# Kernel tuning notes

Hardware: AMD Instinct MI355X
Metric: run time of the kernel (lower is better)

The kernel has to match this reference:

```python
import jax, jax.numpy as jnp
import numpy as np

N = 100000   # nodes
E = 1000000  # edges
F = 128      # num_features
H = 64       # hidden_size
C = 1        # num_classes
G = 128      # num graphs in batch


def gcn_conv(x, W, b, src, dst, deg_inv_sqrt):
    # PyG GCNConv: add self-loops, symmetric normalization D^-1/2 (A+I) D^-1/2, then X W + b
    h = x @ W                                   # [N, H]
    norm = deg_inv_sqrt[src] * deg_inv_sqrt[dst]  # [E]
    msg = h[src] * norm[:, None]                # gather + scale, [E, H]
    out = jnp.zeros_like(h).at[dst].add(msg)    # scatter-add to targets
    out = out + h * (deg_inv_sqrt ** 2)[:, None]  # self-loop contribution
    return out + b


def setup_inputs() -> dict:
    key = jax.random.key(0)
    ks = jax.random.split(key, 12)
    x = jax.random.normal(ks[0], (N, F), dtype=jnp.float32)
    edge_index = jax.random.randint(ks[1], (2, E), 0, N, dtype=jnp.int32).astype(jnp.int64)
    batch = jnp.sort(jax.random.randint(ks[2], (N,), 0, G, dtype=jnp.int32)).astype(jnp.int64)
    def glorot(k, fan_in, fan_out):
        s = np.float32(np.sqrt(6.0 / (fan_in + fan_out)))
        return jax.random.uniform(k, (fan_in, fan_out), jnp.float32, -s, s)
    return {
        "x": x, "edge_index": edge_index, "batch": batch,
        "W1": glorot(ks[3], F, H), "b1": jnp.zeros((H,), jnp.float32),
        "W2": glorot(ks[4], H, H), "b2": jnp.zeros((H,), jnp.float32),
        "Wl1": glorot(ks[5], H, H), "bl1": jnp.zeros((H,), jnp.float32),
        "Wl2": glorot(ks[6], H, C), "bl2": jnp.zeros((C,), jnp.float32),
    }


def reference(x, edge_index, batch, W1, b1, W2, b2, Wl1, bl1, Wl2, bl2):
    src, dst = edge_index[0], edge_index[1]
    # degree with self-loops: 1 + in-degree(target)
    deg = jnp.ones((N,), x.dtype).at[dst].add(jnp.ones((E,), x.dtype))
    deg_inv_sqrt = jax.lax.rsqrt(deg)
    h = jax.nn.relu(gcn_conv(x, W1, b1, src, dst, deg_inv_sqrt))
    h = jax.nn.relu(gcn_conv(h, W2, b2, src, dst, deg_inv_sqrt))
    g = jax.ops.segment_sum(h, batch, num_segments=G)  # global_add_pool, [G, H]
    g = jax.nn.relu(g @ Wl1 + bl1)
    out = g @ Wl2 + bl2                                # [G, 1]
    return out.squeeze(axis=1)                         # [G]
```

## Files before the change

kernel.cpp:

```cpp
#include <hip/hip_runtime.h>

#define NN 100000
#define EE 1000000
#define FF 128
#define HH 64
#define GG 128
#define NB 391
#define MMB 1563
#define GCB 2048

__device__ inline unsigned short f2bf(float f) {
    unsigned u = __float_as_uint(f);
    u += 0x7fffu + ((u >> 16) & 1u);
    return (unsigned short)(u >> 16);
}
__device__ inline float bf2f(unsigned short h) {
    return __uint_as_float((unsigned)h << 16);
}

__global__ void k_hist(const int* __restrict__ ei, int* __restrict__ cnt) {
    int e = blockIdx.x * 256 + threadIdx.x;
    if (e < EE) atomicAdd(&cnt[ei[EE + e]], 1);
}

__global__ void k_scan1(const int* __restrict__ cnt, int* __restrict__ part,
                        float* __restrict__ dis) {
    int i = blockIdx.x * 256 + threadIdx.x;
    int c = (i < NN) ? cnt[i] : 0;
    if (i < NN) dis[i] = rsqrtf((float)(c + 1));
    int v = (i < NN) ? c : 0;
    for (int o = 1; o < 64; o <<= 1) v += __shfl_xor(v, o);
    __shared__ int ws[4];
    if ((threadIdx.x & 63) == 0) ws[threadIdx.x >> 6] = v;
    __syncthreads();
    if (threadIdx.x == 0) part[blockIdx.x] = ws[0] + ws[1] + ws[2] + ws[3];
}

__global__ void k_scan2(int* __restrict__ part) {
    __shared__ int buf[512];
    int t = threadIdx.x;
    int v = (t < NB) ? part[t] : 0;
    buf[t] = v; __syncthreads();
    for (int o = 1; o < 512; o <<= 1) {
        int u = (t >= o) ? buf[t - o] : 0;
        __syncthreads();
        buf[t] += u;
        __syncthreads();
    }
    if (t < NB) part[t] = buf[t] - v;
}

__global__ void k_scan3(const int* __restrict__ cnt, const int* __restrict__ part,
                        int* __restrict__ row_ptr, int* __restrict__ cursor) {
    int i = blockIdx.x * 256 + threadIdx.x;
    int v = (i < NN) ? cnt[i] : 0;
    int lane = threadIdx.x & 63, w = threadIdx.x >> 6;
    int incl = v;
    for (int o = 1; o < 64; o <<= 1) { int u = __shfl_up(incl, o); if (lane >= o) incl += u; }
    __shared__ int ws[4];
    if (lane == 63) ws[w] = incl;
    __syncthreads();
    int woff = 0;
    for (int k = 0; k < w; ++k) woff += ws[k];
    int excl = incl - v + woff + part[blockIdx.x];
    if (i < NN) {
        row_ptr[i] = excl;
        cursor[i]  = excl;
    }
    if (i == 0) row_ptr[NN] = EE;
}

template<int K, int XBF>
__device__ __forceinline__ void
mm_body(const void* __restrict__ Xv, const float* __restrict__ W,
        const float* __restrict__ dis, unsigned* __restrict__ Y8,
        float* __restrict__ S, float* __restrict__ Wl, int bid) {
    for (int i = threadIdx.x; i < K * HH; i += 256) Wl[i] = W[i];
    __syncthreads();
    const int lane = threadIdx.x & 63;
    const int wv   = threadIdx.x >> 6;
    const int c4   = (lane & 15) * 4;
    const int rsg  = lane >> 4;
    const int r0   = bid * 64 + wv * 16 + rsg * 4;

    const char* Xb = (const char*)Xv;
    const size_t rb = (size_t)K * (XBF ? 2 : 4);
    const char* xr0; const char* xr1; const char* xr2; const char* xr3;
    {
        int a = r0, b_ = r0 + 1, c = r0 + 2, d = r0 + 3;
        if (a > NN - 1) a = NN - 1;
        if (b_ > NN - 1) b_ = NN - 1;
        if (c > NN - 1) c = NN - 1;
        if (d > NN - 1) d = NN - 1;
        xr0 = Xb + (size_t)a * rb; xr1 = Xb + (size_t)b_ * rb;
        xr2 = Xb + (size_t)c * rb; xr3 = Xb + (size_t)d * rb;
    }
    float4 acc0 = {0,0,0,0}, acc1 = {0,0,0,0}, acc2 = {0,0,0,0}, acc3 = {0,0,0,0};

#pragma unroll 8
    for (int k4 = 0; k4 < K / 4; ++k4) {
        float4 x0, x1, x2, x3;
        if (XBF) {
            ushort4 u0 = *(const ushort4*)(xr0 + k4 * 8);
            ushort4 u1 = *(const ushort4*)(xr1 + k4 * 8);
            ushort4 u2 = *(const ushort4*)(xr2 + k4 * 8);
            ushort4 u3 = *(const ushort4*)(xr3 + k4 * 8);
            x0 = {bf2f(u0.x), bf2f(u0.y), bf2f(u0.z), bf2f(u0.w)};
            x1 = {bf2f(u1.x), bf2f(u1.y), bf2f(u1.z), bf2f(u1.w)};
            x2 = {bf2f(u2.x), bf2f(u2.y), bf2f(u2.z), bf2f(u2.w)};
            x3 = {bf2f(u3.x), bf2f(u3.y), bf2f(u3.z), bf2f(u3.w)};
        } else {
            x0 = *(const float4*)(xr0 + k4 * 16);
            x1 = *(const float4*)(xr1 + k4 * 16);
            x2 = *(const float4*)(xr2 + k4 * 16);
            x3 = *(const float4*)(xr3 + k4 * 16);
        }
        const float4 w0 = *(const float4*)&Wl[(k4 * 4 + 0) * HH + c4];
        const float4 w1 = *(const float4*)&Wl[(k4 * 4 + 1) * HH + c4];
        const float4 w2 = *(const float4*)&Wl[(k4 * 4 + 2) * HH + c4];
        const float4 w3 = *(const float4*)&Wl[(k4 * 4 + 3) * HH + c4];
#define FMA4(A, XS) \
        A.x = fmaf(XS.x, w0.x, A.x); A.y = fmaf(XS.x, w0.y, A.y); \
        A.z = fmaf(XS.x, w0.z, A.z); A.w = fmaf(XS.x, w0.w, A.w); \
        A.x = fmaf(XS.y, w1.x, A.x); A.y = fmaf(XS.y, w1.y, A.y); \
        A.z = fmaf(XS.y, w1.z, A.z); A.w = fmaf(XS.y, w1.w, A.w); \
        A.x = fmaf(XS.z, w2.x, A.x); A.y = fmaf(XS.z, w2.y, A.y); \
        A.z = fmaf(XS.z, w2.z, A.z); A.w = fmaf(XS.z, w2.w, A.w); \
        A.x = fmaf(XS.w, w3.x, A.x); A.y = fmaf(XS.w, w3.y, A.y); \
        A.z = fmaf(XS.w, w3.z, A.z); A.w = fmaf(XS.w, w3.w, A.w);
        FMA4(acc0, x0) FMA4(acc1, x1) FMA4(acc2, x2) FMA4(acc3, x3)
#undef FMA4
    }
#define STORE(I, A) { \
        const int r = r0 + I; \
        if (r < NN) { \
            const float d = dis[r]; \
            const float ax = A.x * d, ay = A.y * d, az = A.z * d, aw = A.w * d; \
            float m = fmaxf(fmaxf(fabsf(ax), fabsf(ay)), fmaxf(fabsf(az), fabsf(aw))); \
            m = fmaxf(m, __shfl_xor(m, 1)); m = fmaxf(m, __shfl_xor(m, 2)); \
            m = fmaxf(m, __shfl_xor(m, 4)); m = fmaxf(m, __shfl_xor(m, 8)); \
            const float inv = 127.0f / m; \
            int q0 = __float2int_rn(ax * inv), q1 = __float2int_rn(ay * inv); \
            int q2 = __float2int_rn(az * inv), q3 = __float2int_rn(aw * inv); \
            if (m == 0.0f) { q0 = q1 = q2 = q3 = 0; } \
            const unsigned pk = (q0 & 0xff) | ((q1 & 0xff) << 8) | \
                                ((q2 & 0xff) << 16) | ((q3 & 0xff) << 24); \
            Y8[(size_t)r * 16 + (c4 >> 2)] = pk; \
            if (c4 == 0) S[r] = m * (1.0f / 127.0f); \
        } }
    STORE(0, acc0) STORE(1, acc1) STORE(2, acc2) STORE(3, acc3)
#undef STORE
}

template<int K, int XBF>
__global__ __launch_bounds__(256) void
k_matmul_b(const void* __restrict__ X, const float* __restrict__ W,
           const float* __restrict__ dis, unsigned* __restrict__ Y8,
           float* __restrict__ S) {
    __shared__ float Wl[K * HH];
    mm_body<K, XBF>(X, W, dis, Y8, S, Wl, blockIdx.x);
}

__global__ __launch_bounds__(256) void
k_mm1_place(const float* __restrict__ X, const float* __restrict__ W,
            const float* __restrict__ dis, unsigned* __restrict__ Y8,
            float* __restrict__ S, const int* __restrict__ ei,
            int* __restrict__ cursor, int* __restrict__ srcs) {
    __shared__ float Wl[FF * HH];
    if (blockIdx.x < MMB) {
        mm_body<FF, 0>(X, W, dis, Y8, S, Wl, blockIdx.x);
    } else {
        int e = (blockIdx.x - MMB) * 256 + threadIdx.x;
        if (e < EE) {
            int d = ei[EE + e];
            int p = atomicAdd(&cursor[d], 1);
            srcs[p] = ei[e];
        }
    }
}

template<bool POOL>
__global__ __launch_bounds__(256) void
k_gconv(const int* __restrict__ row_ptr, const int* __restrict__ srcs,
        const float* __restrict__ dis, const unsigned* __restrict__ H8,
        const float* __restrict__ S, const float* __restrict__ b,
        unsigned short* __restrict__ Out, const int* __restrict__ batch,
        float* __restrict__ g) {
    const int lane = threadIdx.x & 63;
    const int li   = lane & 15;
    const int qr   = lane >> 4;
    const float bl = b[lane];

    for (int node = blockIdx.x * 4 + (threadIdx.x >> 6); node < NN; node += GCB * 4) {
        const int p0   = row_ptr[node];
        const int deg  = row_ptr[node + 1] - p0;
        const int nbatch = (deg + 8) >> 3;

        float ac0 = 0.f, ac1 = 0.f, ac2 = 0.f, ac3 = 0.f;

#define IDX(bi, dA, dB) { \
        const int iA = 8 * (bi) + qr, iB = iA + 4; \
        dA = __builtin_nontemporal_load(srcs + p0 + (iA < deg ? iA : 0)); \
        dB = __builtin_nontemporal_load(srcs + p0 + (iB < deg ? iB : 0)); }
#define VAL(bi, sA, sB, vA, vB, gA, gB) { \
        const int iA = 8 * (bi) + qr, iB = iA + 4; \
        const int rA = (iA < deg) ? sA : node; \
        const int rB = (iB < deg) ? sB : node; \
        vA = H8[(size_t)rA * 16 + li];  gA = S[rA]; \
        vB = H8[(size_t)rB * 16 + li];  gB = S[rB]; }
#define CONSUME(bi, vA, vB, gA, gB) { \
        const int iA = 8 * (bi) + qr, iB = iA + 4; \
        const float s0 = (iA <= deg) ? gA : 0.f; \
        const float s1 = (iB <= deg) ? gB : 0.f; \
        ac0 = fmaf(s0, (float)(signed char)(vA      ), ac0); \
        ac1 = fmaf(s0, (float)(signed char)(vA >> 8 ), ac1); \
        ac2 = fmaf(s0, (float)(signed char)(vA >> 16), ac2); \
        ac3 = fmaf(s0, (float)(signed char)(vA >> 24), ac3); \
        ac0 = fmaf(s1, (float)(signed char)(vB      ), ac0); \
        ac1 = fmaf(s1, (float)(signed char)(vB >> 8 ), ac1); \
        ac2 = fmaf(s1, (float)(signed char)(vB >> 16), ac2); \
        ac3 = fmaf(s1, (float)(signed char)(vB >> 24), ac3); }

        int sA0, sA1, sB0, sB1;
        unsigned vA0, vA1;
        float gA0, gA1;
        IDX(0, sA0, sA1);
        VAL(0, sA0, sA1, vA0, vA1, gA0, gA1);
        IDX(1, sB0, sB1);
        for (int bi = 1; bi < nbatch; ++bi) {
            unsigned vB0, vB1;
            float gB0, gB1;
            VAL(bi, sB0, sB1, vB0, vB1, gB0, gB1);
            IDX(bi + 1, sB0, sB1);
            CONSUME(bi - 1, vA0, vA1, gA0, gA1);
            vA0 = vB0; vA1 = vB1; gA0 = gB0; gA1 = gB1;
        }
        CONSUME(nbatch - 1, vA0, vA1, gA0, gA1);
#undef IDX
#undef VAL
#undef CONSUME

        ac0 += __shfl_xor(ac0, 16); ac0 += __shfl_xor(ac0, 32);
        ac1 += __shfl_xor(ac1, 16); ac1 += __shfl_xor(ac1, 32);
        ac2 += __shfl_xor(ac2, 16); ac2 += __shfl_xor(ac2, 32);
        ac3 += __shfl_xor(ac3, 16); ac3 += __shfl_xor(ac3, 32);
        const float c0 = __shfl(ac0, lane >> 2);
        const float c1 = __shfl(ac1, lane >> 2);
        const float c2 = __shfl(ac2, lane >> 2);
        const float c3 = __shfl(ac3, lane >> 2);
        const int m = lane & 3;
        const float acc = (m == 0) ? c0 : (m == 1) ? c1 : (m == 2) ? c2 : c3;

        float v = acc * dis[node] + bl;
        v = fmaxf(v, 0.0f);
        if (POOL) {
            unsafeAtomicAdd(&g[(size_t)batch[node] * HH + lane], v);
        } else {
            __builtin_nontemporal_store(f2bf(v), Out + (size_t)node * HH + lane);
        }
    }
}

__global__ void k_head1(const float* __restrict__ g, const float* __restrict__ W,
                        const float* __restrict__ b, float* __restrict__ g2) {
    const int idx = blockIdx.x * 256 + threadIdx.x;
    const int row = idx >> 6;
    const int col = idx & 63;
    const float* gr = g + (size_t)row * HH;
    float acc = b[col];
#pragma unroll
    for (int k = 0; k < HH; ++k) acc = fmaf(gr[k], W[k * HH + col], acc);
    g2[idx] = acc > 0.0f ? acc : 0.0f;
}

__global__ void k_head2(const float* __restrict__ g2, const float* __restrict__ W,
                        const float* __restrict__ b, float* __restrict__ out) {
    const int r = threadIdx.x;
    if (r >= GG) return;
    const float* gr = g2 + (size_t)r * HH;
    float acc = 0.0f;
#pragma unroll
    for (int k = 0; k < HH; ++k) acc = fmaf(gr[k], W[k], acc);
    out[r] = acc + b[0];
}

extern "C" void kernel_launch(void* const* d_in, const int* in_sizes, int n_in,
                              void* d_out, int out_size, void* d_ws, size_t ws_size,
                              hipStream_t stream) {
    const float* x   = (const float*)d_in[0];
    const int*   ei  = (const int*)d_in[1];
    const int*   bat = (const int*)d_in[2];
    const float* W1  = (const float*)d_in[3];
    const float* b1  = (const float*)d_in[4];
    const float* W2  = (const float*)d_in[5];
    const float* b2  = (const float*)d_in[6];
    const float* Wl1 = (const float*)d_in[7];
    const float* bl1 = (const float*)d_in[8];
    const float* Wl2 = (const float*)d_in[9];
    const float* bl2 = (const float*)d_in[10];
    float* out = (float*)d_out;

    char* w = (char*)d_ws;
    float*    dis     = (float*)(w);
    int*      cnt     = (int*)  (w + 400128);
    int*      row_ptr = (int*)  (w + 800256);
    int*      cursor  = (int*)  (w + 1200640);
    int*      part    = (int*)  (w + 1600768);
    int*      srcs    = (int*)  (w + 1602816);
    float*    S       = (float*)(w + 5602816);
    unsigned* H8      = (unsigned*)(w + 6002944);
    unsigned short* A = (unsigned short*)(w + 12402944);
    float*    g       = (float*)(w + 25202944);
    float*    g2      = g + GG * HH;

    hipMemsetAsync(cnt, 0, (size_t)NN * sizeof(int), stream);
    k_hist <<<(EE + 255) / 256, 256, 0, stream>>>(ei, cnt);
    k_scan1<<<NB, 256, 0, stream>>>(cnt, part, dis);
    k_scan2<<<1, 512, 0, stream>>>(part);
    k_scan3<<<NB, 256, 0, stream>>>(cnt, part, row_ptr, cursor);

    k_mm1_place<<<MMB + (EE + 255) / 256, 256, 0, stream>>>(x, W1, dis, H8, S, ei, cursor, srcs);
    k_gconv<false><<<GCB, 256, 0, stream>>>(row_ptr, srcs, dis, H8, S, b1, A, nullptr, nullptr);

    k_matmul_b<HH, 1><<<MMB, 256, 0, stream>>>(A, W2, dis, H8, S);
    hipMemsetAsync(g, 0, (size_t)GG * HH * sizeof(float), stream);
    k_gconv<true><<<GCB, 256, 0, stream>>>(row_ptr, srcs, dis, H8, S, b2, nullptr, bat, g);

    k_head1<<<(GG * HH) / 256, 256, 0, stream>>>(g, Wl1, bl1, g2);
    k_head2<<<1, 128, 0, stream>>>(g2, Wl2, bl2, out);
}
```

Baseline: 280.0 us.

## Split fused matmul/placement kernel and K-tile weights in shared memory

Un-fuses the first matmul from the edge placement pass so each runs as its own kernel, and tiles the weight matrix into 64-row chunks in shared memory (16 KB instead of 32 KB for K=128), which should allow more blocks per CU. It also replaces nontemporal loads/stores in the gather-conv kernel with ordinary cached accesses. The cost is an extra launch, lost overlap between the placement atomics and the matmul, and an extra pair of barriers per K-chunk.

```diff
diff --git a/kernel.cpp b/kernel.cpp
--- a/kernel.cpp
+++ b/kernel.cpp
@@ -70,18 +70,27 @@
     if (i == 0) row_ptr[NN] = EE;
 }
 
+__global__ void k_place(const int* __restrict__ ei, int* __restrict__ cursor,
+                        int* __restrict__ srcs) {
+    int e = blockIdx.x * 256 + threadIdx.x;
+    if (e < EE) {
+        int d = ei[EE + e];
+        int p = atomicAdd(&cursor[d], 1);
+        srcs[p] = ei[e];
+    }
+}
+
 template<int K, int XBF>
-__device__ __forceinline__ void
-mm_body(const void* __restrict__ Xv, const float* __restrict__ W,
-        const float* __restrict__ dis, unsigned* __restrict__ Y8,
-        float* __restrict__ S, float* __restrict__ Wl, int bid) {
-    for (int i = threadIdx.x; i < K * HH; i += 256) Wl[i] = W[i];
-    __syncthreads();
+__global__ __launch_bounds__(256) void
+k_matmul_b(const void* __restrict__ Xv, const float* __restrict__ W,
+           const float* __restrict__ dis, unsigned* __restrict__ Y8,
+           float* __restrict__ S) {
+    __shared__ float Wl[64 * HH];
     const int lane = threadIdx.x & 63;
     const int wv   = threadIdx.x >> 6;
     const int c4   = (lane & 15) * 4;
     const int rsg  = lane >> 4;
-    const int r0   = bid * 64 + wv * 16 + rsg * 4;
+    const int r0   = blockIdx.x * 64 + wv * 16 + rsg * 4;
 
     const char* Xb = (const char*)Xv;
     const size_t rb = (size_t)K * (XBF ? 2 : 4);
@@ -97,39 +106,45 @@
     }
     float4 acc0 = {0,0,0,0}, acc1 = {0,0,0,0}, acc2 = {0,0,0,0}, acc3 = {0,0,0,0};
 
+    for (int ks = 0; ks < K; ks += 64) {
+        __syncthreads();
+        for (int i = threadIdx.x; i < 64 * HH; i += 256) Wl[i] = W[ks * HH + i];
+        __syncthreads();
 #pragma unroll 8
-    for (int k4 = 0; k4 < K / 4; ++k4) {
-        float4 x0, x1, x2, x3;
-        if (XBF) {
-            ushort4 u0 = *(const ushort4*)(xr0 + k4 * 8);
-            ushort4 u1 = *(const ushort4*)(xr1 + k4 * 8);
-            ushort4 u2 = *(const ushort4*)(xr2 + k4 * 8);
-            ushort4 u3 = *(const ushort4*)(xr3 + k4 * 8);
-            x0 = {bf2f(u0.x), bf2f(u0.y), bf2f(u0.z), bf2f(u0.w)};
-            x1 = {bf2f(u1.x), bf2f(u1.y), bf2f(u1.z), bf2f(u1.w)};
-            x2 = {bf2f(u2.x), bf2f(u2.y), bf2f(u2.z), bf2f(u2.w)};
-            x3 = {bf2f(u3.x), bf2f(u3.y), bf2f(u3.z), bf2f(u3.w)};
-        } else {
-            x0 = *(const float4*)(xr0 + k4 * 16);
-            x1 = *(const float4*)(xr1 + k4 * 16);
-            x2 = *(const float4*)(xr2 + k4 * 16);
-            x3 = *(const float4*)(xr3 + k4 * 16);
+        for (int k4 = 0; k4 < 16; ++k4) {
+            const int kk = ks + k4 * 4;
+            float4 x0, x1, x2, x3;
+            if (XBF) {
+                ushort4 u0 = *(const ushort4*)(xr0 + kk * 2);
+                ushort4 u1 = *(const ushort4*)(xr1 + kk * 2);
+                ushort4 u2 = *(const ushort4*)(xr2 + kk * 2);
+                ushort4 u3 = *(const ushort4*)(xr3 + kk * 2);
+                x0 = {bf2f(u0.x), bf2f(u0.y), bf2f(u0.z), bf2f(u0.w)};
+                x1 = {bf2f(u1.x), bf2f(u1.y), bf2f(u1.z), bf2f(u1.w)};
+                x2 = {bf2f(u2.x), bf2f(u2.y), bf2f(u2.z), bf2f(u2.w)};
+                x3 = {bf2f(u3.x), bf2f(u3.y), bf2f(u3.z), bf2f(u3.w)};
+            } else {
+                x0 = *(const float4*)(xr0 + kk * 4);
+                x1 = *(const float4*)(xr1 + kk * 4);
+                x2 = *(const float4*)(xr2 + kk * 4);
+                x3 = *(const float4*)(xr3 + kk * 4);
+            }
+            const float4 w0 = *(const float4*)&Wl[(k4 * 4 + 0) * HH + c4];
+            const float4 w1 = *(const float4*)&Wl[(k4 * 4 + 1) * HH + c4];
+            const float4 w2 = *(const float4*)&Wl[(k4 * 4 + 2) * HH + c4];
+            const float4 w3 = *(const float4*)&Wl[(k4 * 4 + 3) * HH + c4];
+#define FMA4(A, XS) \
+            A.x = fmaf(XS.x, w0.x, A.x); A.y = fmaf(XS.x, w0.y, A.y); \
+            A.z = fmaf(XS.x, w0.z, A.z); A.w = fmaf(XS.x, w0.w, A.w); \
+            A.x = fmaf(XS.y, w1.x, A.x); A.y = fmaf(XS.y, w1.y, A.y); \
+            A.z = fmaf(XS.y, w1.z, A.z); A.w = fmaf(XS.y, w1.w, A.w); \
+            A.x = fmaf(XS.z, w2.x, A.x); A.y = fmaf(XS.z, w2.y, A.y); \
+            A.z = fmaf(XS.z, w2.z, A.z); A.w = fmaf(XS.z, w2.w, A.w); \
+            A.x = fmaf(XS.w, w3.x, A.x); A.y = fmaf(XS.w, w3.y, A.y); \
+            A.z = fmaf(XS.w, w3.z, A.z); A.w = fmaf(XS.w, w3.w, A.w);
+            FMA4(acc0, x0) FMA4(acc1, x1) FMA4(acc2, x2) FMA4(acc3, x3)
+#undef FMA4
         }
-        const float4 w0 = *(const float4*)&Wl[(k4 * 4 + 0) * HH + c4];
-        const float4 w1 = *(const float4*)&Wl[(k4 * 4 + 1) * HH + c4];
-        const float4 w2 = *(const float4*)&Wl[(k4 * 4 + 2) * HH + c4];
-        const float4 w3 = *(const float4*)&Wl[(k4 * 4 + 3) * HH + c4];
-#define FMA4(A, XS) \
-        A.x = fmaf(XS.x, w0.x, A.x); A.y = fmaf(XS.x, w0.y, A.y); \
-        A.z = fmaf(XS.x, w0.z, A.z); A.w = fmaf(XS.x, w0.w, A.w); \
-        A.x = fmaf(XS.y, w1.x, A.x); A.y = fmaf(XS.y, w1.y, A.y); \
-        A.z = fmaf(XS.y, w1.z, A.z); A.w = fmaf(XS.y, w1.w, A.w); \
-        A.x = fmaf(XS.z, w2.x, A.x); A.y = fmaf(XS.z, w2.y, A.y); \
-        A.z = fmaf(XS.z, w2.z, A.z); A.w = fmaf(XS.z, w2.w, A.w); \
-        A.x = fmaf(XS.w, w3.x, A.x); A.y = fmaf(XS.w, w3.y, A.y); \
-        A.z = fmaf(XS.w, w3.z, A.z); A.w = fmaf(XS.w, w3.w, A.w);
-        FMA4(acc0, x0) FMA4(acc1, x1) FMA4(acc2, x2) FMA4(acc3, x3)
-#undef FMA4
     }
 #define STORE(I, A) { \
         const int r = r0 + I; \
@@ -152,33 +167,6 @@
 #undef STORE
 }
 
-template<int K, int XBF>
-__global__ __launch_bounds__(256) void
-k_matmul_b(const void* __restrict__ X, const float* __restrict__ W,
-           const float* __restrict__ dis, unsigned* __restrict__ Y8,
-           float* __restrict__ S) {
-    __shared__ float Wl[K * HH];
-    mm_body<K, XBF>(X, W, dis, Y8, S, Wl, blockIdx.x);
-}
-
-__global__ __launch_bounds__(256) void
-k_mm1_place(const float* __restrict__ X, const float* __restrict__ W,
-            const float* __restrict__ dis, unsigned* __restrict__ Y8,
-            float* __restrict__ S, const int* __restrict__ ei,
-            int* __restrict__ cursor, int* __restrict__ srcs) {
-    __shared__ float Wl[FF * HH];
-    if (blockIdx.x < MMB) {
-        mm_body<FF, 0>(X, W, dis, Y8, S, Wl, blockIdx.x);
-    } else {
-        int e = (blockIdx.x - MMB) * 256 + threadIdx.x;
-        if (e < EE) {
-            int d = ei[EE + e];
-            int p = atomicAdd(&cursor[d], 1);
-            srcs[p] = ei[e];
-        }
-    }
-}
-
 template<bool POOL>
 __global__ __launch_bounds__(256) void
 k_gconv(const int* __restrict__ row_ptr, const int* __restrict__ srcs,
@@ -200,8 +188,8 @@
 
 #define IDX(bi, dA, dB) { \
         const int iA = 8 * (bi) + qr, iB = iA + 4; \
-        dA = __builtin_nontemporal_load(srcs + p0 + (iA < deg ? iA : 0)); \
-        dB = __builtin_nontemporal_load(srcs + p0 + (iB < deg ? iB : 0)); }
+        dA = srcs[p0 + (iA < deg ? iA : 0)]; \
+        dB = srcs[p0 + (iB < deg ? iB : 0)]; }
 #define VAL(bi, sA, sB, vA, vB, gA, gB) { \
         const int iA = 8 * (bi) + qr, iB = iA + 4; \
         const int rA = (iA < deg) ? sA : node; \
@@ -256,7 +244,7 @@
         if (POOL) {
             unsafeAtomicAdd(&g[(size_t)batch[node] * HH + lane], v);
         } else {
-            __builtin_nontemporal_store(f2bf(v), Out + (size_t)node * HH + lane);
+            Out[(size_t)node * HH + lane] = f2bf(v);
         }
     }
 }
@@ -318,8 +306,9 @@
     k_scan1<<<NB, 256, 0, stream>>>(cnt, part, dis);
     k_scan2<<<1, 512, 0, stream>>>(part);
     k_scan3<<<NB, 256, 0, stream>>>(cnt, part, row_ptr, cursor);
-
-    k_mm1_place<<<MMB + (EE + 255) / 256, 256, 0, stream>>>(x, W1, dis, H8, S, ei, cursor, srcs);
+    k_place<<<(EE + 255) / 256, 256, 0, stream>>>(ei, cursor, srcs);
+
+    k_matmul_b<FF, 0><<<MMB, 256, 0, stream>>>(x, W1, dis, H8, S);
     k_gconv<false><<<GCB, 256, 0, stream>>>(row_ptr, srcs, dis, H8, S, b1, A, nullptr, nullptr);
 
     k_matmul_b<HH, 1><<<MMB, 256, 0, stream>>>(A, W2, dis, H8, S);
```

After: 310.4 us. +10.9%, slower.

## Load neighbor list once per wave via shuffle and prefetch next node's indices

Applied to the files above, without the earlier changes.

Each wavefront now loads up to 64 neighbor indices of its node with one coalesced load and hands them out to lanes through shuffles, replacing the per-batch scalar index loads. It also prefetches the next node's row_ptr range and index vector while the current node's last gathers are consumed, so the index latency overlaps across nodes. Nodes with 64 or more neighbors fall back to a simple tail loop, and the output store is no longer nontemporal. The always-two-batch minimum adds some masked dummy gathers for nodes with few neighbors.

```diff
diff --git a/kernel.cpp b/kernel.cpp
--- a/kernel.cpp
+++ b/kernel.cpp
@@ -191,54 +191,70 @@
     const int qr   = lane >> 4;
     const float bl = b[lane];
 
-    for (int node = blockIdx.x * 4 + (threadIdx.x >> 6); node < NN; node += GCB * 4) {
-        const int p0   = row_ptr[node];
-        const int deg  = row_ptr[node + 1] - p0;
-        const int nbatch = (deg + 8) >> 3;
+    int node = __builtin_amdgcn_readfirstlane(blockIdx.x * 4 + (threadIdx.x >> 6));
+    int p0 = row_ptr[node], p1 = row_ptr[node + 1];
+    int idx_l = srcs[p0 + ((lane < p1 - p0) ? lane : 0)];
+
+    while (true) {
+        const int deg = p1 - p0;
+        const int F   = (deg + 1 < 64) ? deg + 1 : 64;
+        int nb = (F + 7) >> 3; if (nb < 2) nb = 2;
 
         float ac0 = 0.f, ac1 = 0.f, ac2 = 0.f, ac3 = 0.f;
-
-#define IDX(bi, dA, dB) { \
+        unsigned uA0, uA1, uB0, uB1;
+        float fA0, fA1, fB0, fB1;
+        int ia, ib;
+
+#define ISSUE(bi, U0, U1, G0, G1) { \
         const int iA = 8 * (bi) + qr, iB = iA + 4; \
-        dA = __builtin_nontemporal_load(srcs + p0 + (iA < deg ? iA : 0)); \
-        dB = __builtin_nontemporal_load(srcs + p0 + (iB < deg ? iB : 0)); }
-#define VAL(bi, sA, sB, vA, vB, gA, gB) { \
-        const int iA = 8 * (bi) + qr, iB = iA + 4; \
+        const int sA = __shfl(idx_l, iA), sB = __shfl(idx_l, iB); \
         const int rA = (iA < deg) ? sA : node; \
         const int rB = (iB < deg) ? sB : node; \
-        vA = H8[(size_t)rA * 16 + li];  gA = S[rA]; \
-        vB = H8[(size_t)rB * 16 + li];  gB = S[rB]; }
-#define CONSUME(bi, vA, vB, gA, gB) { \
+        U0 = H8[(size_t)rA * 16 + li];  G0 = S[rA]; \
+        U1 = H8[(size_t)rB * 16 + li];  G1 = S[rB]; }
+#define CONS(bi, U0, U1, G0, G1) { \
         const int iA = 8 * (bi) + qr, iB = iA + 4; \
-        const float s0 = (iA <= deg) ? gA : 0.f; \
-        const float s1 = (iB <= deg) ? gB : 0.f; \
-        ac0 = fmaf(s0, (float)(signed char)(vA      ), ac0); \
-        ac1 = fmaf(s0, (float)(signed char)(vA >> 8 ), ac1); \
-        ac2 = fmaf(s0, (float)(signed char)(vA >> 16), ac2); \
-        ac3 = fmaf(s0, (float)(signed char)(vA >> 24), ac3); \
-        ac0 = fmaf(s1, (float)(signed char)(vB      ), ac0); \
-        ac1 = fmaf(s1, (float)(signed char)(vB >> 8 ), ac1); \
-        ac2 = fmaf(s1, (float)(signed char)(vB >> 16), ac2); \
-        ac3 = fmaf(s1, (float)(signed char)(vB >> 24), ac3); }
-
-        int sA0, sA1, sB0, sB1;
-        unsigned vA0, vA1;
-        float gA0, gA1;
-        IDX(0, sA0, sA1);
-        VAL(0, sA0, sA1, vA0, vA1, gA0, gA1);
-        IDX(1, sB0, sB1);
-        for (int bi = 1; bi < nbatch; ++bi) {
-            unsigned vB0, vB1;
-            float gB0, gB1;
-            VAL(bi, sB0, sB1, vB0, vB1, gB0, gB1);
-            IDX(bi + 1, sB0, sB1);
-            CONSUME(bi - 1, vA0, vA1, gA0, gA1);
-            vA0 = vB0; vA1 = vB1; gA0 = gB0; gA1 = gB1;
-        }
-        CONSUME(nbatch - 1, vA0, vA1, gA0, gA1);
-#undef IDX
-#undef VAL
-#undef CONSUME
+        const float s0 = (iA <= deg) ? G0 : 0.f; \
+        const float s1 = (iB <= deg) ? G1 : 0.f; \
+        ac0 = fmaf(s0, (float)(signed char)(U0      ), ac0); \
+        ac1 = fmaf(s0, (float)(signed char)(U0 >> 8 ), ac1); \
+        ac2 = fmaf(s0, (float)(signed char)(U0 >> 16), ac2); \
+        ac3 = fmaf(s0, (float)(signed char)(U0 >> 24), ac3); \
+        ac0 = fmaf(s1, (float)(signed char)(U1      ), ac0); \
+        ac1 = fmaf(s1, (float)(signed char)(U1 >> 8 ), ac1); \
+        ac2 = fmaf(s1, (float)(signed char)(U1 >> 16), ac2); \
+        ac3 = fmaf(s1, (float)(signed char)(U1 >> 24), ac3); }
+
+        ISSUE(0, uA0, uA1, fA0, fA1) ia = 0;
+        ISSUE(1, uB0, uB1, fB0, fB1) ib = 1;
+        for (int bi = 2; bi < nb; ++bi) {
+            CONS(ia, uA0, uA1, fA0, fA1)
+            uA0 = uB0; uA1 = uB1; fA0 = fB0; fA1 = fB1; ia = ib;
+            ISSUE(bi, uB0, uB1, fB0, fB1) ib = bi;
+        }
+
+        const int nnode = node + GCB * 4;
+        int np0 = 0, np1 = 0, nidx = 0;
+        if (nnode < NN) {
+            np0 = row_ptr[nnode]; np1 = row_ptr[nnode + 1];
+            nidx = srcs[np0 + ((lane < np1 - np0) ? lane : 0)];
+        }
+
+        CONS(ia, uA0, uA1, fA0, fA1)
+        CONS(ib, uB0, uB1, fB0, fB1)
+#undef ISSUE
+#undef CONS
+        if (deg >= 64) {
+            for (int i = 64 + qr; i <= deg; i += 4) {
+                const int r = (i < deg) ? srcs[p0 + i] : node;
+                const unsigned v = H8[(size_t)r * 16 + li];
+                const float s = S[r];
+                ac0 = fmaf(s, (float)(signed char)(v      ), ac0);
+                ac1 = fmaf(s, (float)(signed char)(v >> 8 ), ac1);
+                ac2 = fmaf(s, (float)(signed char)(v >> 16), ac2);
+                ac3 = fmaf(s, (float)(signed char)(v >> 24), ac3);
+            }
+        }
 
         ac0 += __shfl_xor(ac0, 16); ac0 += __shfl_xor(ac0, 32);
         ac1 += __shfl_xor(ac1, 16); ac1 += __shfl_xor(ac1, 32);
@@ -256,8 +272,11 @@
         if (POOL) {
             unsafeAtomicAdd(&g[(size_t)batch[node] * HH + lane], v);
         } else {
-            __builtin_nontemporal_store(f2bf(v), Out + (size_t)node * HH + lane);
-        }
+            Out[(size_t)node * HH + lane] = f2bf(v);
+        }
+
+        if (nnode >= NN) break;
+        node = nnode; p0 = np0; p1 = np1; idx_l = nidx;
     }
 }
 
```

New measurement: 271.7 us, median of 2. 1.03x faster.
